# Optimization experiments

Hardware: AMD Instinct MI355X
Metric: run time of the kernel (lower is better)

Reference implementation:

```python
import jax, jax.numpy as jnp
import numpy as np

DIM = 512
NUM_HEADS = 8
HEAD_DIM = DIM // NUM_HEADS
GAMMA = 1.0


def setup_inputs() -> dict:
    key = jax.random.key(0)
    ks = jax.random.split(key, 10)
    B, S = 2, 2048
    x_real = jax.random.normal(ks[0], (B, S, DIM), dtype=jnp.float32)
    x_imag = jax.random.normal(ks[1], (B, S, DIM), dtype=jnp.float32)
    def xavier(k, fan_in, fan_out):
        lim = float(np.sqrt(6.0 / (fan_in + fan_out)))
        return jax.random.uniform(k, (fan_in, fan_out), jnp.float32, -lim, lim)
    # torch Linear(in,out): weight [out,in]; we store transposed [in,out]
    Wq = xavier(ks[2], 2 * DIM, DIM); bq = jnp.zeros((DIM,), jnp.float32)
    Wk = xavier(ks[3], 2 * DIM, DIM); bk = jnp.zeros((DIM,), jnp.float32)
    Wv = xavier(ks[4], 2 * DIM, DIM); bv = jnp.zeros((DIM,), jnp.float32)
    Wo = xavier(ks[5], DIM, 2 * DIM); bo = jnp.zeros((2 * DIM,), jnp.float32)
    return {"x_real": x_real, "x_imag": x_imag, "Wq": Wq, "bq": bq,
            "Wk": Wk, "bk": bk, "Wv": Wv, "bv": bv, "Wo": Wo, "bo": bo}


def reference(x_real, x_imag, Wq, bq, Wk, bk, Wv, bv, Wo, bo):
    B, S, _ = x_real.shape
    real_embed = jnp.concatenate([x_real, x_imag], axis=-1)  # [B,S,2*dim]
    def proj(W, b):
        y = real_embed @ W + b                               # [B,S,dim]
        return y.reshape(B, S, NUM_HEADS, HEAD_DIM).transpose(0, 2, 1, 3)  # [B,H,S,d]
    Q = proj(Wq, bq)
    K = proj(Wk, bk)
    V = proj(Wv, bv)
    # softmax over head_dim is broadcast-invariant, so the Bhattacharyya
    # coefficient sum_d sqrt(p_i[d]*q_j[d]) factorizes into a matmul.
    sp = jnp.sqrt(jax.nn.softmax(Q, axis=-1))  # [B,H,S,d]
    sq = jnp.sqrt(jax.nn.softmax(K, axis=-1))  # [B,H,S,d]
    bc = jnp.einsum('bhid,bhjd->bhij', sp, sq)  # Bhattacharyya coeff [B,H,S,S]
    bc = jnp.clip(bc, -1.0, 1.0)
    dist = jnp.arccos(bc)
    attn = jax.nn.softmax(-GAMMA * dist * dist, axis=-1)  # [B,H,S,S]
    attended = jnp.einsum('bhij,bhjd->bhid', attn, V)
    attended = attended.transpose(0, 2, 1, 3).reshape(B, S, DIM)
    out = attended @ Wo + bo  # [B,S,2*dim] = concat(real_out, imag_out)
    return out
```

## Files before the change

kernel.cpp:

```cpp
#include <hip/hip_runtime.h>
#include <math.h>


typedef __attribute__((ext_vector_type(8))) short short8;
typedef __attribute__((ext_vector_type(4))) short bf16x4;
typedef __attribute__((ext_vector_type(4))) float f32x4;
typedef __attribute__((ext_vector_type(2))) float f32x2;
typedef __attribute__((ext_vector_type(4))) unsigned int u32x4;

#define MFMA(a, b, c) __builtin_amdgcn_mfma_f32_16x16x32_bf16((a), (b), (c), 0, 0, 0)

static __device__ __forceinline__ short f2bf(float f) {
    unsigned u = __float_as_uint(f);
    u += 0x7fffu + ((u >> 16) & 1u);
    return (short)(u >> 16);
}

static __device__ __forceinline__ void gld_lds16(const short* g, short* l) {
    __builtin_amdgcn_global_load_lds(
        (const __attribute__((address_space(1))) unsigned int*)g,
        (__attribute__((address_space(3))) unsigned int*)l, 16, 0, 0);
}

__global__ __launch_bounds__(256) void convert_x(
    const float* __restrict__ xr, const float* __restrict__ xi,
    short* __restrict__ xb)
{
    int idx = blockIdx.x * 256 + threadIdx.x;
    int e = idx << 2;
    int m = e >> 10, k = e & 1023;
    const float* src = (k < 512) ? xr : xi;
    float4 t = *(const float4*)(src + (size_t)m * 512 + (k & 511));
    unsigned lo = (unsigned short)f2bf(t.x) | ((unsigned)(unsigned short)f2bf(t.y) << 16);
    unsigned hi = (unsigned short)f2bf(t.z) | ((unsigned)(unsigned short)f2bf(t.w) << 16);
    uint2 o; o.x = lo; o.y = hi;
    *(uint2*)(xb + e) = o;
}

__global__ __launch_bounds__(256) void transpose_w(
    const float* __restrict__ Wq, const float* __restrict__ Wk,
    const float* __restrict__ Wv, const float* __restrict__ Wo,
    short* __restrict__ wqt, short* __restrict__ wkt,
    short* __restrict__ wvt, short* __restrict__ wot)
{
    __shared__ float t[32][33];
    const int z = blockIdx.z;
    const float* src = (z == 0) ? Wq : (z == 1) ? Wk : (z == 2) ? Wv : Wo;
    short* dst = (z == 0) ? wqt : (z == 1) ? wkt : (z == 2) ? wvt : wot;
    const int K = (z < 3) ? 1024 : 512;
    const int N = (z < 3) ? 512 : 1024;
    const int n0 = blockIdx.x << 5, k0 = blockIdx.y << 5;
    if (n0 >= N || k0 >= K) return;
    const int tx = threadIdx.x & 31, ty = threadIdx.x >> 5;
    #pragma unroll
    for (int i = 0; i < 4; ++i)
        t[ty + 8 * i][tx] = src[(size_t)(k0 + ty + 8 * i) * N + n0 + tx];
    __syncthreads();
    #pragma unroll
    for (int i = 0; i < 4; ++i)
        dst[(size_t)(n0 + ty + 8 * i) * K + k0 + tx] = f2bf(t[tx][ty + 8 * i]);
}

__global__ __launch_bounds__(64) void qkv_mfma(
    const short* __restrict__ xb, const short* __restrict__ wcat,
    const float* __restrict__ bq, const float* __restrict__ bk,
    const float* __restrict__ bv,
    short* __restrict__ sp, short* __restrict__ sq, short* __restrict__ vt)
{
    __shared__ short As[3][64 * 32];
    __shared__ short Bs[3][64 * 32];
    const int jb = blockIdx.x;
    const int m0 = blockIdx.y << 6;
    const int lane = threadIdx.x;
    const int l = lane & 15, quad = lane >> 4;

    const int srow = lane >> 2;
    const int sseg = (lane & 3) << 3;
    const short* gA = xb   + (size_t)(m0        + srow) * 1024 + sseg;
    const short* gB = wcat + (size_t)((jb << 6) + srow) * 1024 + sseg;

    auto STAGE = [&](int bb, int kk) {
        const int k0 = kk << 5;
        #pragma unroll
        for (int t = 0; t < 4; ++t) {
            gld_lds16(gA + k0 + t * 16 * 1024, &As[bb][t << 9]);
            gld_lds16(gB + k0 + t * 16 * 1024, &Bs[bb][t << 9]);
        }
    };

    STAGE(0, 0);
    STAGE(1, 1);
    asm volatile("s_waitcnt vmcnt(8)" ::: "memory");

    const f32x4 z4 = {0.f, 0.f, 0.f, 0.f};
    f32x4 acc[4][4];
    #pragma unroll
    for (int i = 0; i < 4; ++i)
        #pragma unroll
        for (int j = 0; j < 4; ++j) acc[i][j] = z4;

    int cb = 0, sb = 2;
    #pragma unroll 1
    for (int kt = 0; kt < 32; ++kt) {
        STAGE(sb, (kt + 2) & 31);
        const short* Al = &As[cb][0];
        const short* Bl = &Bs[cb][0];
        short8 af[4], bfr[4];
        #pragma unroll
        for (int i = 0; i < 4; ++i)
            af[i] = *(const short8*)(Al + (((i << 4) + l) << 5) + (quad << 3));
        #pragma unroll
        for (int j = 0; j < 4; ++j)
            bfr[j] = *(const short8*)(Bl + (((j << 4) + l) << 5) + (quad << 3));
        #pragma unroll
        for (int i = 0; i < 4; ++i)
            #pragma unroll
            for (int j = 0; j < 4; ++j)
                acc[i][j] = MFMA(af[i], bfr[j], acc[i][j]);
        asm volatile("s_waitcnt vmcnt(8)" ::: "memory");
        cb = (cb == 2) ? 0 : cb + 1;
        sb = (sb == 2) ? 0 : sb + 1;
    }

    const int op = jb >> 3;
    const int h  = jb & 7;

    if (op < 2) {
        short* dst = (op == 0) ? sp : sq;
        const float* bias = (op == 0) ? bq : bk;
        float bcol[4];
        #pragma unroll
        for (int nt = 0; nt < 4; ++nt) bcol[nt] = bias[(h << 6) + (nt << 4) + l];
        #pragma unroll
        for (int i = 0; i < 4; ++i) {
            #pragma unroll
            for (int reg = 0; reg < 4; ++reg) {
                const int r = m0 + (i << 4) + (quad << 2) + reg;
                const int b = r >> 11, s = r & 2047;
                float v[4];
                #pragma unroll
                for (int nt = 0; nt < 4; ++nt) v[nt] = acc[i][nt][reg] + bcol[nt];
                float mx = fmaxf(fmaxf(v[0], v[1]), fmaxf(v[2], v[3]));
                #pragma unroll
                for (int msk = 1; msk < 16; msk <<= 1) mx = fmaxf(mx, __shfl_xor(mx, msk));
                float e[4], ssum = 0.f;
                #pragma unroll
                for (int nt = 0; nt < 4; ++nt) { e[nt] = __expf(v[nt] - mx); ssum += e[nt]; }
                #pragma unroll
                for (int msk = 1; msk < 16; msk <<= 1) ssum += __shfl_xor(ssum, msk);
                float inv = 1.0f / ssum;
                short* o = dst + ((size_t)((b << 3) + h) * 2048 + s) * 64 + l;
                #pragma unroll
                for (int nt = 0; nt < 4; ++nt)
                    o[nt << 4] = f2bf(sqrtf(e[nt] * inv));
            }
        }
    } else {
        float bcol[4];
        #pragma unroll
        for (int nt = 0; nt < 4; ++nt) bcol[nt] = bv[(h << 6) + (nt << 4) + l];
        #pragma unroll
        for (int i = 0; i < 4; ++i) {
            const int sb2 = m0 + (i << 4) + (quad << 2);
            const int b = sb2 >> 11, s = sb2 & 2047;
            #pragma unroll
            for (int nt = 0; nt < 4; ++nt) {
                const int d = (nt << 4) + l;
                bf16x4 pk;
                #pragma unroll
                for (int reg = 0; reg < 4; ++reg)
                    pk[reg] = f2bf(acc[i][nt][reg] + bcol[nt]);
                *(bf16x4*)(vt + ((size_t)((b << 3) + h) * 64 + d) * 2048 + s) = pk;
            }
        }
    }
}

__global__ __launch_bounds__(256, 4) void attn_mfma(
    const short* __restrict__ sp, const short* __restrict__ sq,
    const short* __restrict__ vt,
    float* __restrict__ pnum, float* __restrict__ pden)
{
    __shared__ __align__(16) short sqT[2][64 * 64];
    __shared__ __align__(16) short vtT[2][64 * 64];
    const int bh = blockIdx.y;
    const int m0 = blockIdx.x << 6;
    const int z  = blockIdx.z;
    const int tid = threadIdx.x;
    const int w = tid >> 6, lane = tid & 63;
    const int l = lane & 15, quad = lane >> 4;
    const int l7 = l & 7;

    const short* spB = sp + (size_t)bh * 2048 * 64;
    const short* sqB = sq + (size_t)bh * 2048 * 64;
    const short* vtB = vt + (size_t)bh * 64 * 2048;

    const short* apr = spB + (size_t)(m0 + w * 16 + l) * 64 + quad * 8;
    short8 nq0 = (*(const short8*)(apr)) ^ (short)0x8000;
    short8 nq1 = (*(const short8*)(apr + 32)) ^ (short)0x8000;

    const int srow = tid >> 2;
    const int t3 = tid & 3;
    const int scol = t3 * 16;
    const short* sqG = sqB + (size_t)srow * 64 + scol;
    const short* vtG = vtB + (size_t)srow * 2048 + scol;
    const int sl0 = t3 << 1;
    const int sw0 = srow * 64 + (((sl0    ) ^ (srow & 7)) << 3);
    const int sw1 = srow * 64 + (((sl0 | 1) ^ (srow & 7)) << 3);
    int vwo[4];
    #pragma unroll
    for (int m = 0; m < 4; ++m)
        vwo[m] = srow * 64 + ((((t3 >> 1) * 4 + m) ^ (srow & 7)) << 3)
               + ((t3 & 1) << 2);

    const int sRd = (quad ^ l7) << 3;

    {
        const int j0 = (z << 4) << 6;
        short8 a0 = *(const short8*)(sqG + (size_t)j0 * 64);
        short8 a1 = *(const short8*)(sqG + (size_t)j0 * 64 + 8);
        short8 b0 = *(const short8*)(vtG + j0);
        short8 b1 = *(const short8*)(vtG + j0 + 8);
        *(short8*)(&sqT[0][sw0]) = a0;
        *(short8*)(&sqT[0][sw1]) = a1;
        u32x4 u0 = __builtin_bit_cast(u32x4, b0);
        u32x4 u1 = __builtin_bit_cast(u32x4, b1);
        *(uint2*)(&vtT[0][vwo[0]]) = (uint2){u0.x, u0.y};
        *(uint2*)(&vtT[0][vwo[1]]) = (uint2){u0.z, u0.w};
        *(uint2*)(&vtT[0][vwo[2]]) = (uint2){u1.x, u1.y};
        *(uint2*)(&vtT[0][vwo[3]]) = (uint2){u1.z, u1.w};
    }
    __syncthreads();

    const f32x4 ones4 = {1.f, 1.f, 1.f, 1.f};
    const f32x4 z4 = {0.f, 0.f, 0.f, 0.f};
    f32x4 acc[4] = {z4, z4, z4, z4};
    f32x2 den2 = {0.f, 0.f};

    #pragma unroll 1
    for (int jtl = 0; jtl < 16; ++jtl) {
        const int cb = jtl & 1, nb = cb ^ 1;
        const int j0n = ((z << 4) + ((jtl + 1) & 15)) << 6;
        short8 na0 = *(const short8*)(sqG + (size_t)j0n * 64);
        short8 na1 = *(const short8*)(sqG + (size_t)j0n * 64 + 8);
        short8 nb0 = *(const short8*)(vtG + j0n);
        short8 nb1 = *(const short8*)(vtG + j0n + 8);

        uint2 pk[4];
        const short* sqL = &sqT[cb][0];
        #pragma unroll
        for (int nt = 0; nt < 4; ++nt) {
            const short* ar = sqL + ((nt * 16 + l) << 6);
            short8 sa0 = *(const short8*)(ar + sRd);
            short8 sa1 = *(const short8*)(ar + (sRd ^ 32));
            f32x4 p = MFMA(sa0, nq0, ones4);
            p = MFMA(sa1, nq1, p);
            f32x2 u01 = {p[0], p[1]};
            f32x2 u23 = {p[2], p[3]};
            const f32x2 zz = {0.f, 0.f};
#if __has_builtin(__builtin_elementwise_max)
            u01 = __builtin_elementwise_max(u01, zz);
            u23 = __builtin_elementwise_max(u23, zz);
#else
            u01.x = fmaxf(u01.x, 0.f); u01.y = fmaxf(u01.y, 0.f);
            u23.x = fmaxf(u23.x, 0.f); u23.y = fmaxf(u23.y, 0.f);
#endif
            f32x2 t01 = {-0.00133017f, -0.00133017f};
            f32x2 t23 = t01;
            t01 = t01 * u01 - 0.00219618f;  t23 = t23 * u23 - 0.00219618f;
            t01 = t01 * u01 - 0.00555151f;  t23 = t23 * u23 - 0.00555151f;
            t01 = t01 * u01 - 0.01465597f;  t23 = t23 * u23 - 0.01465597f;
            t01 = t01 * u01 - 0.04121986f;  t23 = t23 * u23 - 0.04121986f;
            t01 = t01 * u01 - 0.12823956f;  t23 = t23 * u23 - 0.12823956f;
            t01 = t01 * u01 - 0.48089834f;  t23 = t23 * u23 - 0.48089834f;
            t01 = t01 * u01 - 2.88539008f;  t23 = t23 * u23 - 2.88539008f;
            f32x2 w01 = u01 * t01;
            f32x2 w23 = u23 * t23;
#if __has_builtin(__builtin_amdgcn_exp2f)
            float e0 = __builtin_amdgcn_exp2f(w01.x);
            float e1 = __builtin_amdgcn_exp2f(w01.y);
            float e2 = __builtin_amdgcn_exp2f(w23.x);
            float e3 = __builtin_amdgcn_exp2f(w23.y);
#else
            float e0 = exp2f(w01.x), e1 = exp2f(w01.y);
            float e2 = exp2f(w23.x), e3 = exp2f(w23.y);
#endif
            f32x2 es = {e0 + e2, e1 + e3};
            den2 += es;
            pk[nt].x = (__float_as_uint(e0) >> 16) | (__float_as_uint(e1) & 0xffff0000u);
            pk[nt].y = (__float_as_uint(e2) >> 16) | (__float_as_uint(e3) & 0xffff0000u);
        }

        u32x4 c0; c0.x = pk[0].x; c0.y = pk[0].y; c0.z = pk[1].x; c0.w = pk[1].y;
        u32x4 c1; c1.x = pk[2].x; c1.y = pk[2].y; c1.z = pk[3].x; c1.w = pk[3].y;
        short8 pa0 = __builtin_bit_cast(short8, c0);
        short8 pa1 = __builtin_bit_cast(short8, c1);
        const short* vL = &vtT[cb][0];
        #pragma unroll
        for (int t4 = 0; t4 < 4; ++t4) {
            const short* vr = vL + ((t4 * 16 + l) << 6);
            short8 vb0 = *(const short8*)(vr + sRd);
            short8 vb1 = *(const short8*)(vr + (sRd ^ 32));
            acc[t4] = MFMA(pa0, vb0, acc[t4]);
            acc[t4] = MFMA(pa1, vb1, acc[t4]);
        }

        *(short8*)(&sqT[nb][sw0]) = na0;
        *(short8*)(&sqT[nb][sw1]) = na1;
        u32x4 u0 = __builtin_bit_cast(u32x4, nb0);
        u32x4 u1 = __builtin_bit_cast(u32x4, nb1);
        *(uint2*)(&vtT[nb][vwo[0]]) = (uint2){u0.x, u0.y};
        *(uint2*)(&vtT[nb][vwo[1]]) = (uint2){u0.z, u0.w};
        *(uint2*)(&vtT[nb][vwo[2]]) = (uint2){u1.x, u1.y};
        *(uint2*)(&vtT[nb][vwo[3]]) = (uint2){u1.z, u1.w};
        __syncthreads();
    }

    float den = den2.x + den2.y;
    den += __shfl_xor(den, 16);
    den += __shfl_xor(den, 32);
    if (lane < 16)
        pden[(size_t)z * 32768 + bh * 2048 + m0 + w * 16 + l] = den;

    const int b = bh >> 3, hh = bh & 7;
    float* np = pnum + (size_t)z * 4096 * 512;
    #pragma unroll
    for (int t4 = 0; t4 < 4; ++t4)
        #pragma unroll
        for (int reg = 0; reg < 4; ++reg) {
            const int row = m0 + w * 16 + quad * 4 + reg;
            np[((size_t)(b * 2048 + row)) * 512 + hh * 64 + t4 * 16 + l] =
                acc[t4][reg];
        }
}

__global__ __launch_bounds__(256) void combine_attn(
    const float* __restrict__ pnum, const float* __restrict__ pden,
    short* __restrict__ attB)
{
    const int idx = (blockIdx.x * 256 + threadIdx.x) << 3;
    const int r = idx >> 9;
    const int c = idx & 511;
    const int hh = c >> 6;
    const int bh = ((r >> 11) << 3) + hh;
    const int srow = r & 2047;
    const float d = pden[bh * 2048 + srow] + pden[32768 + bh * 2048 + srow];
    const float inv = 1.0f / d;
    const float* n0 = pnum + (size_t)r * 512 + c;
    const float* n1 = n0 + (size_t)4096 * 512;
    float4 a0 = *(const float4*)(n0);
    float4 a1 = *(const float4*)(n0 + 4);
    float4 b0 = *(const float4*)(n1);
    float4 b1 = *(const float4*)(n1 + 4);
    short8 o;
    o[0] = f2bf((a0.x + b0.x) * inv);
    o[1] = f2bf((a0.y + b0.y) * inv);
    o[2] = f2bf((a0.z + b0.z) * inv);
    o[3] = f2bf((a0.w + b0.w) * inv);
    o[4] = f2bf((a1.x + b1.x) * inv);
    o[5] = f2bf((a1.y + b1.y) * inv);
    o[6] = f2bf((a1.z + b1.z) * inv);
    o[7] = f2bf((a1.w + b1.w) * inv);
    *(short8*)(attB + idx) = o;
}

__global__ __launch_bounds__(64) void out_mfma(
    const short* __restrict__ attB, const short* __restrict__ wot,
    const float* __restrict__ bo, float* __restrict__ out)
{
    __shared__ short As[3][64 * 32];
    __shared__ short Bs[3][64 * 32];
    const int n0 = blockIdx.x << 6;
    const int m0 = blockIdx.y << 6;
    const int lane = threadIdx.x;
    const int l = lane & 15, quad = lane >> 4;

    const int srow = lane >> 2;
    const int sseg = (lane & 3) << 3;
    const short* gA = attB + (size_t)(m0 + srow) * 512 + sseg;
    const short* gB = wot  + (size_t)(n0 + srow) * 512 + sseg;

    auto STAGE = [&](int bb, int kk) {
        const int k0 = kk << 5;
        #pragma unroll
        for (int t = 0; t < 4; ++t) {
            gld_lds16(gA + k0 + t * 16 * 512, &As[bb][t << 9]);
            gld_lds16(gB + k0 + t * 16 * 512, &Bs[bb][t << 9]);
        }
    };

    STAGE(0, 0);
    STAGE(1, 1);
    asm volatile("s_waitcnt vmcnt(8)" ::: "memory");

    const f32x4 z4 = {0.f, 0.f, 0.f, 0.f};
    f32x4 acc[4][4];
    #pragma unroll
    for (int i = 0; i < 4; ++i)
        #pragma unroll
        for (int j = 0; j < 4; ++j) acc[i][j] = z4;

    int cb = 0, sb = 2;
    #pragma unroll 1
    for (int kt = 0; kt < 16; ++kt) {
        STAGE(sb, (kt + 2) & 15);
        const short* Al = &As[cb][0];
        const short* Bl = &Bs[cb][0];
        short8 af[4], bfr[4];
        #pragma unroll
        for (int i = 0; i < 4; ++i)
            af[i] = *(const short8*)(Al + (((i << 4) + l) << 5) + (quad << 3));
        #pragma unroll
        for (int j = 0; j < 4; ++j)
            bfr[j] = *(const short8*)(Bl + (((j << 4) + l) << 5) + (quad << 3));
        #pragma unroll
        for (int i = 0; i < 4; ++i)
            #pragma unroll
            for (int j = 0; j < 4; ++j)
                acc[i][j] = MFMA(af[i], bfr[j], acc[i][j]);
        asm volatile("s_waitcnt vmcnt(8)" ::: "memory");
        cb = (cb == 2) ? 0 : cb + 1;
        sb = (sb == 2) ? 0 : sb + 1;
    }

    float bcol[4];
    #pragma unroll
    for (int nt = 0; nt < 4; ++nt) bcol[nt] = bo[n0 + (nt << 4) + l];
    #pragma unroll
    for (int i = 0; i < 4; ++i)
        #pragma unroll
        for (int reg = 0; reg < 4; ++reg) {
            const int m = m0 + (i << 4) + (quad << 2) + reg;
            float* o = out + (size_t)m * 1024 + n0 + l;
            #pragma unroll
            for (int nt = 0; nt < 4; ++nt)
                o[nt << 4] = acc[i][nt][reg] + bcol[nt];
        }
}

extern "C" void kernel_launch(void* const* d_in, const int* in_sizes, int n_in,
                              void* d_out, int out_size, void* d_ws, size_t ws_size,
                              hipStream_t stream) {
    const float* xr = (const float*)d_in[0];
    const float* xi = (const float*)d_in[1];
    const float* Wq = (const float*)d_in[2];
    const float* bq = (const float*)d_in[3];
    const float* Wk = (const float*)d_in[4];
    const float* bk = (const float*)d_in[5];
    const float* Wv = (const float*)d_in[6];
    const float* bv = (const float*)d_in[7];
    const float* Wo = (const float*)d_in[8];
    const float* bo = (const float*)d_in[9];
    float* out = (float*)d_out;

    short* base = (short*)d_ws;
    short* xb   = base;
    short* wqt  = xb  + 4194304;
    short* wkt  = wqt + 524288;
    short* wvt  = wkt + 524288;
    short* wot  = wvt + 524288;
    short* spW  = wot + 524288;
    short* sqW  = spW + 2097152;
    short* vtW  = sqW + 2097152;
    short* attB = vtW + 2097152;
    float* pnum = (float*)(attB + 2097152);
    float* pden = pnum + 8388608;

    hipLaunchKernelGGL(convert_x, dim3(4096), dim3(256), 0, stream, xr, xi, xb);
    hipLaunchKernelGGL(transpose_w, dim3(32, 32, 4), dim3(256), 0, stream,
                       Wq, Wk, Wv, Wo, wqt, wkt, wvt, wot);
    hipLaunchKernelGGL(qkv_mfma, dim3(24, 64), dim3(64), 0, stream,
                       xb, wqt, bq, bk, bv, spW, sqW, vtW);
    hipLaunchKernelGGL(attn_mfma, dim3(32, 16, 2), dim3(256), 0, stream,
                       spW, sqW, vtW, pnum, pden);
    hipLaunchKernelGGL(combine_attn, dim3(1024), dim3(256), 0, stream,
                       pnum, pden, attB);
    hipLaunchKernelGGL(out_mfma, dim3(16, 64), dim3(64), 0, stream,
                       attB, wot, bo, out);
}
```

Before: 180.2 us.

## Pre-swizzle K and V layouts in projection kernel; use direct global-to-LDS loads in attention

```diff
diff --git a/kernel.cpp b/kernel.cpp
--- a/kernel.cpp
+++ b/kernel.cpp
@@ -73,6 +73,7 @@
     const int m0 = blockIdx.y << 6;
     const int lane = threadIdx.x;
     const int l = lane & 15, quad = lane >> 4;
+    const int l7 = l & 7;
 
     const int srow = lane >> 2;
     const int sseg = (lane & 3) << 3;
@@ -149,10 +150,18 @@
                 #pragma unroll
                 for (int msk = 1; msk < 16; msk <<= 1) ssum += __shfl_xor(ssum, msk);
                 float inv = 1.0f / ssum;
-                short* o = dst + ((size_t)((b << 3) + h) * 2048 + s) * 64 + l;
-                #pragma unroll
-                for (int nt = 0; nt < 4; ++nt)
-                    o[nt << 4] = f2bf(sqrtf(e[nt] * inv));
+                short* o = dst + ((size_t)((b << 3) + h) * 2048 + s) * 64;
+                if (op == 0) {
+                    #pragma unroll
+                    for (int nt = 0; nt < 4; ++nt)
+                        o[(nt << 4) + l] = f2bf(sqrtf(e[nt] * inv));
+                } else {
+                    const int s7 = r & 7;
+                    #pragma unroll
+                    for (int nt = 0; nt < 4; ++nt)
+                        o[((((nt << 1) + (l >> 3)) ^ s7) << 3) + l7] =
+                            f2bf(sqrtf(e[nt] * inv));
+                }
             }
         }
     } else {
@@ -163,6 +172,9 @@
         for (int i = 0; i < 4; ++i) {
             const int sb2 = m0 + (i << 4) + (quad << 2);
             const int b = sb2 >> 11, s = sb2 & 2047;
+            const int gg = (s >> 2) & 15;
+            const int u = ((gg >> 3) << 2) + (gg & 3);
+            const int colp = (s & ~63) + (((u ^ l7)) << 3) + (((gg >> 2) & 1) << 2);
             #pragma unroll
             for (int nt = 0; nt < 4; ++nt) {
                 const int d = (nt << 4) + l;
@@ -170,7 +182,7 @@
                 #pragma unroll
                 for (int reg = 0; reg < 4; ++reg)
                     pk[reg] = f2bf(acc[i][nt][reg] + bcol[nt]);
-                *(bf16x4*)(vt + ((size_t)((b << 3) + h) * 64 + d) * 2048 + s) = pk;
+                *(bf16x4*)(vt + ((size_t)((b << 3) + h) * 64 + d) * 2048 + colp) = pk;
             }
         }
     }
@@ -199,37 +211,24 @@
     short8 nq0 = (*(const short8*)(apr)) ^ (short)0x8000;
     short8 nq1 = (*(const short8*)(apr + 32)) ^ (short)0x8000;
 
-    const int srow = tid >> 2;
-    const int t3 = tid & 3;
-    const int scol = t3 * 16;
-    const short* sqG = sqB + (size_t)srow * 64 + scol;
-    const short* vtG = vtB + (size_t)srow * 2048 + scol;
-    const int sl0 = t3 << 1;
-    const int sw0 = srow * 64 + (((sl0    ) ^ (srow & 7)) << 3);
-    const int sw1 = srow * 64 + (((sl0 | 1) ^ (srow & 7)) << 3);
-    int vwo[4];
-    #pragma unroll
-    for (int m = 0; m < 4; ++m)
-        vwo[m] = srow * 64 + ((((t3 >> 1) * 4 + m) ^ (srow & 7)) << 3)
-               + ((t3 & 1) << 2);
+    const int lr = lane >> 3;
+    const int lu = lane & 7;
+    const int r0 = w << 1;
+
+    auto STAGEATT = [&](int buf, int jrow) {
+        #pragma unroll
+        for (int k = 0; k < 2; ++k) {
+            const int r = r0 + k;
+            gld_lds16(sqB + (size_t)(jrow + (r << 3) + lr) * 64 + (lu << 3),
+                      &sqT[buf][r << 9]);
+            gld_lds16(vtB + (size_t)((r << 3) + lr) * 2048 + jrow + (lu << 3),
+                      &vtT[buf][r << 9]);
+        }
+    };
 
     const int sRd = (quad ^ l7) << 3;
 
-    {
-        const int j0 = (z << 4) << 6;
-        short8 a0 = *(const short8*)(sqG + (size_t)j0 * 64);
-        short8 a1 = *(const short8*)(sqG + (size_t)j0 * 64 + 8);
-        short8 b0 = *(const short8*)(vtG + j0);
-        short8 b1 = *(const short8*)(vtG + j0 + 8);
-        *(short8*)(&sqT[0][sw0]) = a0;
-        *(short8*)(&sqT[0][sw1]) = a1;
-        u32x4 u0 = __builtin_bit_cast(u32x4, b0);
-        u32x4 u1 = __builtin_bit_cast(u32x4, b1);
-        *(uint2*)(&vtT[0][vwo[0]]) = (uint2){u0.x, u0.y};
-        *(uint2*)(&vtT[0][vwo[1]]) = (uint2){u0.z, u0.w};
-        *(uint2*)(&vtT[0][vwo[2]]) = (uint2){u1.x, u1.y};
-        *(uint2*)(&vtT[0][vwo[3]]) = (uint2){u1.z, u1.w};
-    }
+    STAGEATT(0, z << 10);
     __syncthreads();
 
     const f32x4 ones4 = {1.f, 1.f, 1.f, 1.f};
@@ -240,11 +239,8 @@
     #pragma unroll 1
     for (int jtl = 0; jtl < 16; ++jtl) {
         const int cb = jtl & 1, nb = cb ^ 1;
-        const int j0n = ((z << 4) + ((jtl + 1) & 15)) << 6;
-        short8 na0 = *(const short8*)(sqG + (size_t)j0n * 64);
-        short8 na1 = *(const short8*)(sqG + (size_t)j0n * 64 + 8);
-        short8 nb0 = *(const short8*)(vtG + j0n);
-        short8 nb1 = *(const short8*)(vtG + j0n + 8);
+        const int j0n = (z << 10) + (((jtl + 1) & 15) << 6);
+        STAGEATT(nb, j0n);
 
         uint2 pk[4];
         const short* sqL = &sqT[cb][0];
@@ -305,14 +301,6 @@
             acc[t4] = MFMA(pa1, vb1, acc[t4]);
         }
 
-        *(short8*)(&sqT[nb][sw0]) = na0;
-        *(short8*)(&sqT[nb][sw1]) = na1;
-        u32x4 u0 = __builtin_bit_cast(u32x4, nb0);
-        u32x4 u1 = __builtin_bit_cast(u32x4, nb1);
-        *(uint2*)(&vtT[nb][vwo[0]]) = (uint2){u0.x, u0.y};
-        *(uint2*)(&vtT[nb][vwo[1]]) = (uint2){u0.z, u0.w};
-        *(uint2*)(&vtT[nb][vwo[2]]) = (uint2){u1.x, u1.y};
-        *(uint2*)(&vtT[nb][vwo[3]]) = (uint2){u1.z, u1.w};
         __syncthreads();
     }
 
```

Measured after the change: 187.5 us. 1.04x slower.
